# Kernel tuning notes

Measured on AMD Instinct MI355X. Metric: run time of the kernel, lower is better.

The kernel has to match this reference:

```python
import jax, jax.numpy as jnp
import numpy as np

B, S, H, E, K, D = 1, 4096, 1024, 8, 2, 2048

def setup_inputs() -> dict:
    key = jax.random.key(0)
    k1, k2, k3, k4, k5 = jax.random.split(key, 5)
    x = jax.random.normal(k1, (B, S, H), dtype=jnp.float32)
    attention_mask = jnp.ones((B, S), dtype=jnp.int32)
    expert_weights = jax.random.uniform(k2, (B, S, K), dtype=jnp.float32)
    # distinct top-K expert indices per token (torch code requires at most one match per token)
    r = jax.random.uniform(k3, (B, S, E))
    chosen_expert_indices = jnp.argsort(r, axis=-1)[..., :K].astype(jnp.int64)
    down_proj = jax.random.normal(k4, (E, H, D), dtype=jnp.float32)
    up_proj = jax.random.normal(k5, (E, D, H), dtype=jnp.float32)
    return {"x": x, "attention_mask": attention_mask, "expert_weights": expert_weights,
            "chosen_expert_indices": chosen_expert_indices, "down_proj": down_proj, "up_proj": up_proj}

def reference(x, attention_mask, expert_weights, chosen_expert_indices, down_proj, up_proj):
    b, s, h = x.shape
    e = down_proj.shape[0]
    xt = x.reshape(-1, h)                                   # [N,H]
    n = xt.shape[0]
    mask = attention_mask.reshape(n, 1).astype(x.dtype)     # [N,1]
    idx = chosen_expert_indices.reshape(n, -1)              # [N,K]
    w = expert_weights.reshape(n, -1)                       # [N,K]
    onehot = jax.nn.one_hot(idx, e, dtype=x.dtype)          # [N,K,E]
    # per-token routing weight for each expert (0 if not chosen), masked
    we = jnp.einsum('nk,nke->ne', w, onehot) * mask         # [N,E]
    hid = jax.nn.relu(jnp.einsum('nh,ehd->end', xt, down_proj))  # [E,N,D]
    y = jnp.einsum('end,edh->enh', hid, up_proj)            # [E,N,H]
    mlp = jnp.einsum('ne,enh->nh', we, y)                   # [N,H]
    out = xt + mlp                                          # residual (B==1 as in source)
    return out.reshape(b, s, h)
```

## Files before the change

### kernel.cpp

```cpp
#include <hip/hip_runtime.h>
#include <stdint.h>

#define NTOK 4096
#define HDIM 1024
#define DDIM 2048
#define NEXP 8
#define NASS 8192

typedef __attribute__((ext_vector_type(8))) short bf16x8;
typedef __attribute__((ext_vector_type(4))) float f32x4;

typedef __attribute__((address_space(1))) const unsigned int gu32;
typedef __attribute__((address_space(3))) unsigned int lu32;

#define BARRIER() asm volatile("s_barrier" ::: "memory")
#define WAIT_VM0() asm volatile("s_waitcnt vmcnt(0)" ::: "memory")

__device__ __forceinline__ void async16(void* lds, const void* g) {
  __builtin_amdgcn_global_load_lds((gu32*)(uintptr_t)g, (lu32*)(uintptr_t)lds, 16, 0, 0);
}

__device__ __forceinline__ unsigned short f2bf(float f) {
  unsigned int u = __float_as_uint(f);
  return (unsigned short)((u + 0x7fffu + ((u >> 16) & 1u)) >> 16);
}
__device__ __forceinline__ float bf2f(unsigned short u) {
  return __uint_as_float(((unsigned int)u) << 16);
}

__global__ __launch_bounds__(256) void k_cvt_x(const float* __restrict__ x,
                                               unsigned short* __restrict__ x16) {
  int i = blockIdx.x * 256 + threadIdx.x;
  float4 v = reinterpret_cast<const float4*>(x)[i];
  ushort4 o;
  o.x = f2bf(v.x); o.y = f2bf(v.y); o.z = f2bf(v.z); o.w = f2bf(v.w);
  reinterpret_cast<ushort4*>(x16)[i] = o;
}

__global__ __launch_bounds__(256) void k_transpose(const float* __restrict__ in,
                                                   unsigned short* __restrict__ out,
                                                   int R, int C) {
  __shared__ float t[32][33];
  const size_t mbase = (size_t)blockIdx.z * R * C;
  int tid = threadIdx.x;
  int r = tid >> 3, c4 = (tid & 7) * 4;
  int gr = blockIdx.y * 32 + r;
  int gc = blockIdx.x * 32 + c4;
  float4 v = *reinterpret_cast<const float4*>(in + mbase + (size_t)gr * C + gc);
  t[r][c4 + 0] = v.x; t[r][c4 + 1] = v.y; t[r][c4 + 2] = v.z; t[r][c4 + 3] = v.w;
  __syncthreads();
  int orow = blockIdx.x * 32 + r;
  int oc4  = blockIdx.y * 32 + c4;
  ushort4 o;
  o.x = f2bf(t[c4 + 0][r]); o.y = f2bf(t[c4 + 1][r]);
  o.z = f2bf(t[c4 + 2][r]); o.w = f2bf(t[c4 + 3][r]);
  *reinterpret_cast<ushort4*>(out + mbase + (size_t)orow * R + oc4) = o;
}

__global__ __launch_bounds__(1024) void k_route(
    const int* __restrict__ idx, const float* __restrict__ ew,
    const int* __restrict__ amask,
    int* __restrict__ counts_g, int* __restrict__ offs_g,
    int* __restrict__ toks, float* __restrict__ wl, int* __restrict__ slotmap) {
  __shared__ int cnt[NEXP], cur[NEXP], flag;
  const int t = threadIdx.x;
  if (t < NEXP) cnt[t] = 0;
  if (t == 0) flag = 0;
  __syncthreads();
  int lf = 0;
#pragma unroll
  for (int j = 0; j < 4; ++j) {
    int i = t + j * 1024;
    if (idx[2 * i + 1] != 0) lf = 1;
  }
  if (lf) atomicOr(&flag, 1);
  __syncthreads();
  const int is32 = flag;
  int e[8];
#pragma unroll
  for (int j = 0; j < 8; ++j) {
    int i = t + j * 1024;
    int ei = is32 ? idx[i] : idx[2 * i];
    e[j] = ei;
    atomicAdd(&cnt[ei], 1);
  }
  __syncthreads();
  if (t == 0) {
    int off = 0;
    for (int k = 0; k < NEXP; ++k) {
      cur[k] = off; offs_g[k] = off; counts_g[k] = cnt[k]; off += cnt[k];
    }
  }
  __syncthreads();
#pragma unroll
  for (int j = 0; j < 8; ++j) {
    int i = t + j * 1024;
    int n = i >> 1;
    int slot = atomicAdd(&cur[e[j]], 1);
    toks[slot] = n;
    wl[slot] = ew[i] * (amask[n] ? 1.0f : 0.0f);
    slotmap[i] = slot;
  }
}

__global__ __launch_bounds__(512, 4) void k_down_fused(
    const unsigned short* __restrict__ x16, const unsigned short* __restrict__ bT,
    const int* __restrict__ counts, const int* __restrict__ offs,
    const int* __restrict__ toks, unsigned short* __restrict__ hid,
    const float* __restrict__ up, unsigned short* __restrict__ upT) {
  const int e = blockIdx.x;
  const int q = blockIdx.y;
  const int tid = threadIdx.x;
  __shared__ alignas(16) char lds[65536];

  if (q >= 1024) {
    const int tt = (q - 1024) * 2 + (tid >> 8);
    const int bx = tt & 31;
    const int by = tt >> 5;
    float* tb = (float*)lds + (tid >> 8) * (32 * 33);
    const int t2 = tid & 255;
    const int r = t2 >> 3, c4 = (t2 & 7) * 4;
    const size_t mbase = (size_t)e * DDIM * HDIM;
    const int gr = by * 32 + r;
    const int gc = bx * 32 + c4;
    float4 v = *reinterpret_cast<const float4*>(up + mbase + (size_t)gr * HDIM + gc);
    tb[r * 33 + c4 + 0] = v.x; tb[r * 33 + c4 + 1] = v.y;
    tb[r * 33 + c4 + 2] = v.z; tb[r * 33 + c4 + 3] = v.w;
    __syncthreads();
    const int orow = bx * 32 + r;
    const int oc4  = by * 32 + c4;
    ushort4 o;
    o.x = f2bf(tb[(c4 + 0) * 33 + r]); o.y = f2bf(tb[(c4 + 1) * 33 + r]);
    o.z = f2bf(tb[(c4 + 2) * 33 + r]); o.w = f2bf(tb[(c4 + 3) * 33 + r]);
    *reinterpret_cast<ushort4*>(upT + mbase + (size_t)orow * DDIM + oc4) = o;
    return;
  }

  const int cnt = counts[e];
  const int mt = q >> 4;
  const int nt = q & 15;
  if (mt * 128 >= cnt) return;
  const int base = offs[e];
  const int lane = tid & 63;
  const int wr = ((tid >> 8) & 1) * 64;
  const int wc = ((tid >> 6) & 3) * 32;

  const char* gA[2]; const char* gB[2]; int sOff[2];
  {
    const int swcol = ((tid & 7) << 4) ^ (((tid >> 3) & 7) << 4);
#pragma unroll
    for (int it = 0; it < 2; ++it) {
      int row = it * 64 + (tid >> 3);
      int sl = mt * 128 + row; if (sl >= cnt) sl = cnt - 1;
      gA[it] = (const char*)(x16 + (size_t)toks[base + sl] * HDIM) + swcol;
      gB[it] = (const char*)(bT + (size_t)e * DDIM * HDIM + (size_t)(nt * 128 + row) * HDIM) + swcol;
      sOff[it] = it * 8192 + tid * 16;
    }
  }
  const int swz = (lane & 7) << 4;
  const int lo = (lane >> 4) << 4;
  int rowA[4], rowB[2];
#pragma unroll
  for (int m = 0; m < 4; ++m) rowA[m] = (wr + m * 16 + (lane & 15)) * 128;
#pragma unroll
  for (int n = 0; n < 2; ++n) rowB[n] = (wc + n * 16 + (lane & 15)) * 128;

#pragma unroll
  for (int it = 0; it < 2; ++it) {
    async16(lds + sOff[it], gA[it]);
    async16(lds + 32768 + sOff[it], gB[it]);
  }
  WAIT_VM0();
  BARRIER();

  f32x4 acc[4][2] = {};
  for (int j = 0; j < 16; ++j) {
    char* curA = lds + ((j & 1) << 14);
    char* curB = lds + 32768 + ((j & 1) << 14);
    char* nxtA = lds + ((~j & 1) << 14);
    char* nxtB = lds + 32768 + ((~j & 1) << 14);
    bf16x8 fa0[4], fb0[2], fa1[4], fb1[2];
    {
      const int cx = lo ^ swz;
#pragma unroll
      for (int m = 0; m < 4; ++m) fa0[m] = *reinterpret_cast<const bf16x8*>(curA + rowA[m] + cx);
#pragma unroll
      for (int n = 0; n < 2; ++n) fb0[n] = *reinterpret_cast<const bf16x8*>(curB + rowB[n] + cx);
    }
    if (j < 15) {
      const int ko = (j + 1) << 7;
#pragma unroll
      for (int it = 0; it < 2; ++it) {
        async16(nxtA + sOff[it], gA[it] + ko);
        async16(nxtB + sOff[it], gB[it] + ko);
      }
    }
    {
      const int cx = (64 | lo) ^ swz;
#pragma unroll
      for (int m = 0; m < 4; ++m) fa1[m] = *reinterpret_cast<const bf16x8*>(curA + rowA[m] + cx);
#pragma unroll
      for (int n = 0; n < 2; ++n) fb1[n] = *reinterpret_cast<const bf16x8*>(curB + rowB[n] + cx);
    }
#pragma unroll
    for (int m = 0; m < 4; ++m)
#pragma unroll
      for (int n = 0; n < 2; ++n)
        acc[m][n] = __builtin_amdgcn_mfma_f32_16x16x32_bf16(fa0[m], fb0[n], acc[m][n], 0, 0, 0);
#pragma unroll
    for (int m = 0; m < 4; ++m)
#pragma unroll
      for (int n = 0; n < 2; ++n)
        acc[m][n] = __builtin_amdgcn_mfma_f32_16x16x32_bf16(fa1[m], fb1[n], acc[m][n], 0, 0, 0);
    WAIT_VM0();
    BARRIER();
  }

#pragma unroll
  for (int m = 0; m < 4; ++m) {
    int r0 = mt * 128 + wr + m * 16 + ((lane >> 4) * 4);
#pragma unroll
    for (int j = 0; j < 4; ++j) {
      int r = r0 + j;
      if (r < cnt) {
        unsigned short* dst = hid + (size_t)(base + r) * DDIM + nt * 128 + wc + (lane & 15);
#pragma unroll
        for (int n = 0; n < 2; ++n) {
          float v = acc[m][n][j];
          dst[n * 16] = f2bf(v > 0.f ? v : 0.f);
        }
      }
    }
  }
}

__global__ __launch_bounds__(512, 4) void k_gemm_up(
    const unsigned short* __restrict__ hid, const unsigned short* __restrict__ bT,
    const int* __restrict__ counts, const int* __restrict__ offs,
    unsigned short* __restrict__ yw) {
  const int e = blockIdx.x;
  const int cnt = counts[e];
  const int q = blockIdx.y;
  const int mt = q >> 3;
  const int nt = q & 7;
  if (mt * 128 >= cnt) return;
  const int base = offs[e];
  __shared__ alignas(16) char lds[65536];
  const int tid = threadIdx.x;
  const int lane = tid & 63;
  const int wr = ((tid >> 8) & 1) * 64;
  const int wc = ((tid >> 6) & 3) * 32;

  const char* gA[2]; const char* gB[2]; int sOff[2];
  {
    const int swcol = ((tid & 7) << 4) ^ (((tid >> 3) & 7) << 4);
#pragma unroll
    for (int it = 0; it < 2; ++it) {
      int row = it * 64 + (tid >> 3);
      int sl = mt * 128 + row; if (sl >= cnt) sl = cnt - 1;
      gA[it] = (const char*)(hid + (size_t)(base + sl) * DDIM) + swcol;
      gB[it] = (const char*)(bT + (size_t)e * HDIM * DDIM + (size_t)(nt * 128 + row) * DDIM) + swcol;
      sOff[it] = it * 8192 + tid * 16;
    }
  }
  const int swz = (lane & 7) << 4;
  const int lo = (lane >> 4) << 4;
  int rowA[4], rowB[2];
#pragma unroll
  for (int m = 0; m < 4; ++m) rowA[m] = (wr + m * 16 + (lane & 15)) * 128;
#pragma unroll
  for (int n = 0; n < 2; ++n) rowB[n] = (wc + n * 16 + (lane & 15)) * 128;

#pragma unroll
  for (int it = 0; it < 2; ++it) {
    async16(lds + sOff[it], gA[it]);
    async16(lds + 32768 + sOff[it], gB[it]);
  }
  WAIT_VM0();
  BARRIER();

  f32x4 acc[4][2] = {};
  for (int j = 0; j < 32; ++j) {
    char* curA = lds + ((j & 1) << 14);
    char* curB = lds + 32768 + ((j & 1) << 14);
    char* nxtA = lds + ((~j & 1) << 14);
    char* nxtB = lds + 32768 + ((~j & 1) << 14);
    bf16x8 fa0[4], fb0[2], fa1[4], fb1[2];
    {
      const int cx = lo ^ swz;
#pragma unroll
      for (int m = 0; m < 4; ++m) fa0[m] = *reinterpret_cast<const bf16x8*>(curA + rowA[m] + cx);
#pragma unroll
      for (int n = 0; n < 2; ++n) fb0[n] = *reinterpret_cast<const bf16x8*>(curB + rowB[n] + cx);
    }
    if (j < 31) {
      const int ko = (j + 1) << 7;
#pragma unroll
      for (int it = 0; it < 2; ++it) {
        async16(nxtA + sOff[it], gA[it] + ko);
        async16(nxtB + sOff[it], gB[it] + ko);
      }
    }
    {
      const int cx = (64 | lo) ^ swz;
#pragma unroll
      for (int m = 0; m < 4; ++m) fa1[m] = *reinterpret_cast<const bf16x8*>(curA + rowA[m] + cx);
#pragma unroll
      for (int n = 0; n < 2; ++n) fb1[n] = *reinterpret_cast<const bf16x8*>(curB + rowB[n] + cx);
    }
#pragma unroll
    for (int m = 0; m < 4; ++m)
#pragma unroll
      for (int n = 0; n < 2; ++n)
        acc[m][n] = __builtin_amdgcn_mfma_f32_16x16x32_bf16(fa0[m], fb0[n], acc[m][n], 0, 0, 0);
#pragma unroll
    for (int m = 0; m < 4; ++m)
#pragma unroll
      for (int n = 0; n < 2; ++n)
        acc[m][n] = __builtin_amdgcn_mfma_f32_16x16x32_bf16(fa1[m], fb1[n], acc[m][n], 0, 0, 0);
    WAIT_VM0();
    BARRIER();
  }

#pragma unroll
  for (int m = 0; m < 4; ++m) {
    int r0 = mt * 128 + wr + m * 16 + ((lane >> 4) * 4);
#pragma unroll
    for (int j = 0; j < 4; ++j) {
      int r = r0 + j;
      if (r < cnt) {
        unsigned short* dst = yw + (size_t)(base + r) * HDIM + nt * 128 + wc + (lane & 15);
#pragma unroll
        for (int n = 0; n < 2; ++n) dst[n * 16] = f2bf(acc[m][n][j]);
      }
    }
  }
}

__global__ __launch_bounds__(256) void k_combine(
    const float* __restrict__ x, const unsigned short* __restrict__ yw,
    const int* __restrict__ slotmap, const float* __restrict__ wl,
    float* __restrict__ out) {
  const int n = blockIdx.x;
  const int t = threadIdx.x;
  const int s0 = slotmap[2 * n], s1 = slotmap[2 * n + 1];
  const float w0 = wl[s0], w1 = wl[s1];
  float4 xv = reinterpret_cast<const float4*>(x + (size_t)n * HDIM)[t];
  ushort4 a0 = reinterpret_cast<const ushort4*>(yw + (size_t)s0 * HDIM)[t];
  ushort4 b0 = reinterpret_cast<const ushort4*>(yw + (size_t)s1 * HDIM)[t];
  float4 r;
  r.x = xv.x + w0 * bf2f(a0.x) + w1 * bf2f(b0.x);
  r.y = xv.y + w0 * bf2f(a0.y) + w1 * bf2f(b0.y);
  r.z = xv.z + w0 * bf2f(a0.z) + w1 * bf2f(b0.z);
  r.w = xv.w + w0 * bf2f(a0.w) + w1 * bf2f(b0.w);
  reinterpret_cast<float4*>(out + (size_t)n * HDIM)[t] = r;
}

extern "C" void kernel_launch(void* const* d_in, const int* in_sizes, int n_in,
                              void* d_out, int out_size, void* d_ws, size_t ws_size,
                              hipStream_t stream) {
  const float* x    = (const float*)d_in[0];
  const int* amask  = (const int*)d_in[1];
  const float* ew   = (const float*)d_in[2];
  const int* cidx   = (const int*)d_in[3];
  const float* dn   = (const float*)d_in[4];
  const float* up   = (const float*)d_in[5];
  float* out        = (float*)d_out;
  char* ws          = (char*)d_ws;

  const size_t X16_OFF = 0;
  const size_t DNT_OFF = X16_OFF + (size_t)NTOK * HDIM * 2;
  const size_t UPT_OFF = DNT_OFF + (size_t)NEXP * HDIM * DDIM * 2;
  const size_t HID_OFF = UPT_OFF + (size_t)NEXP * HDIM * DDIM * 2;
  const size_t MET_OFF = HID_OFF + (size_t)NASS * DDIM * 2;

  unsigned short* x16 = (unsigned short*)(ws + X16_OFF);
  unsigned short* dnT = (unsigned short*)(ws + DNT_OFF);
  unsigned short* upT = (unsigned short*)(ws + UPT_OFF);
  unsigned short* hid = (unsigned short*)(ws + HID_OFF);
  unsigned short* yw  = (unsigned short*)(ws + DNT_OFF);
  int* counts  = (int*)(ws + MET_OFF);
  int* offs    = counts + 8;
  int* toks    = counts + 32;
  float* wl    = (float*)(toks + NASS);
  int* slotmap = (int*)(wl + NASS);

  k_cvt_x<<<NTOK * HDIM / 1024, 256, 0, stream>>>(x, x16);
  k_transpose<<<dim3(DDIM / 32, HDIM / 32, NEXP), 256, 0, stream>>>(dn, dnT, HDIM, DDIM);
  k_route<<<1, 1024, 0, stream>>>(cidx, ew, amask, counts, offs, toks, wl, slotmap);
  k_down_fused<<<dim3(8, 2048), 512, 0, stream>>>(x16, dnT, counts, offs, toks, hid,
                                                  up, upT);
  k_gemm_up<<<dim3(8, 512), 512, 0, stream>>>(hid, upT, counts, offs, yw);
  k_combine<<<NTOK, 256, 0, stream>>>(x, yw, slotmap, wl, out);
}
```

Before: 159.8 us.

## Triple-buffer GEMM K-loop with prefetch depth two and unfuse up-proj transpose

Both expert GEMM kernels move from a double-buffered LDS pipeline that waited for all loads at the end of each iteration to a three-stage ring. Loads are issued two k-steps ahead and the wait uses vmcnt(4), so memory latency can overlap more of the MFMA work. LDS per block grows to 96KB and launch bounds drop to two blocks per CU, which lowers occupancy. The up_proj transpose that had been fused into the down GEMM launch now runs as its own transpose kernel, so it no longer overlaps with the GEMM.

```diff
diff --git a/kernel.cpp b/kernel.cpp
--- a/kernel.cpp
+++ b/kernel.cpp
@@ -14,7 +14,6 @@
 typedef __attribute__((address_space(3))) unsigned int lu32;
 
 #define BARRIER() asm volatile("s_barrier" ::: "memory")
-#define WAIT_VM0() asm volatile("s_waitcnt vmcnt(0)" ::: "memory")
 
 __device__ __forceinline__ void async16(void* lds, const void* g) {
   __builtin_amdgcn_global_load_lds((gu32*)(uintptr_t)g, (lu32*)(uintptr_t)lds, 16, 0, 0);
@@ -103,44 +102,19 @@
   }
 }
 
-__global__ __launch_bounds__(512, 4) void k_down_fused(
+__global__ __launch_bounds__(512, 2) void k_gemm_down(
     const unsigned short* __restrict__ x16, const unsigned short* __restrict__ bT,
     const int* __restrict__ counts, const int* __restrict__ offs,
-    const int* __restrict__ toks, unsigned short* __restrict__ hid,
-    const float* __restrict__ up, unsigned short* __restrict__ upT) {
+    const int* __restrict__ toks, unsigned short* __restrict__ hid) {
   const int e = blockIdx.x;
+  const int cnt = counts[e];
   const int q = blockIdx.y;
-  const int tid = threadIdx.x;
-  __shared__ alignas(16) char lds[65536];
-
-  if (q >= 1024) {
-    const int tt = (q - 1024) * 2 + (tid >> 8);
-    const int bx = tt & 31;
-    const int by = tt >> 5;
-    float* tb = (float*)lds + (tid >> 8) * (32 * 33);
-    const int t2 = tid & 255;
-    const int r = t2 >> 3, c4 = (t2 & 7) * 4;
-    const size_t mbase = (size_t)e * DDIM * HDIM;
-    const int gr = by * 32 + r;
-    const int gc = bx * 32 + c4;
-    float4 v = *reinterpret_cast<const float4*>(up + mbase + (size_t)gr * HDIM + gc);
-    tb[r * 33 + c4 + 0] = v.x; tb[r * 33 + c4 + 1] = v.y;
-    tb[r * 33 + c4 + 2] = v.z; tb[r * 33 + c4 + 3] = v.w;
-    __syncthreads();
-    const int orow = bx * 32 + r;
-    const int oc4  = by * 32 + c4;
-    ushort4 o;
-    o.x = f2bf(tb[(c4 + 0) * 33 + r]); o.y = f2bf(tb[(c4 + 1) * 33 + r]);
-    o.z = f2bf(tb[(c4 + 2) * 33 + r]); o.w = f2bf(tb[(c4 + 3) * 33 + r]);
-    *reinterpret_cast<ushort4*>(upT + mbase + (size_t)orow * DDIM + oc4) = o;
-    return;
-  }
-
-  const int cnt = counts[e];
   const int mt = q >> 4;
   const int nt = q & 15;
   if (mt * 128 >= cnt) return;
   const int base = offs[e];
+  __shared__ alignas(16) char lds[98304];
+  const int tid = threadIdx.x;
   const int lane = tid & 63;
   const int wr = ((tid >> 8) & 1) * 64;
   const int wc = ((tid >> 6) & 3) * 32;
@@ -168,17 +142,32 @@
 #pragma unroll
   for (int it = 0; it < 2; ++it) {
     async16(lds + sOff[it], gA[it]);
-    async16(lds + 32768 + sOff[it], gB[it]);
-  }
-  WAIT_VM0();
-  BARRIER();
+    async16(lds + 49152 + sOff[it], gB[it]);
+  }
+#pragma unroll
+  for (int it = 0; it < 2; ++it) {
+    async16(lds + 16384 + sOff[it], gA[it] + 128);
+    async16(lds + 49152 + 16384 + sOff[it], gB[it] + 128);
+  }
 
   f32x4 acc[4][2] = {};
+  int cj = 0, sj = 2;
   for (int j = 0; j < 16; ++j) {
-    char* curA = lds + ((j & 1) << 14);
-    char* curB = lds + 32768 + ((j & 1) << 14);
-    char* nxtA = lds + ((~j & 1) << 14);
-    char* nxtB = lds + 32768 + ((~j & 1) << 14);
+    if (j < 15) { asm volatile("s_waitcnt vmcnt(4)" ::: "memory"); }
+    else        { asm volatile("s_waitcnt vmcnt(0)" ::: "memory"); }
+    BARRIER();
+    if (j + 2 < 16) {
+      const int ko = (j + 2) << 7;
+      char* sA = lds + sj * 16384;
+      char* sB = lds + 49152 + sj * 16384;
+#pragma unroll
+      for (int it = 0; it < 2; ++it) {
+        async16(sA + sOff[it], gA[it] + ko);
+        async16(sB + sOff[it], gB[it] + ko);
+      }
+    }
+    char* curA = lds + cj * 16384;
+    char* curB = lds + 49152 + cj * 16384;
     bf16x8 fa0[4], fb0[2], fa1[4], fb1[2];
     {
       const int cx = lo ^ swz;
@@ -187,14 +176,6 @@
 #pragma unroll
       for (int n = 0; n < 2; ++n) fb0[n] = *reinterpret_cast<const bf16x8*>(curB + rowB[n] + cx);
     }
-    if (j < 15) {
-      const int ko = (j + 1) << 7;
-#pragma unroll
-      for (int it = 0; it < 2; ++it) {
-        async16(nxtA + sOff[it], gA[it] + ko);
-        async16(nxtB + sOff[it], gB[it] + ko);
-      }
-    }
     {
       const int cx = (64 | lo) ^ swz;
 #pragma unroll
@@ -212,8 +193,8 @@
 #pragma unroll
       for (int n = 0; n < 2; ++n)
         acc[m][n] = __builtin_amdgcn_mfma_f32_16x16x32_bf16(fa1[m], fb1[n], acc[m][n], 0, 0, 0);
-    WAIT_VM0();
-    BARRIER();
+    cj = (cj == 2) ? 0 : cj + 1;
+    sj = (sj == 2) ? 0 : sj + 1;
   }
 
 #pragma unroll
@@ -234,7 +215,7 @@
   }
 }
 
-__global__ __launch_bounds__(512, 4) void k_gemm_up(
+__global__ __launch_bounds__(512, 2) void k_gemm_up(
     const unsigned short* __restrict__ hid, const unsigned short* __restrict__ bT,
     const int* __restrict__ counts, const int* __restrict__ offs,
     unsigned short* __restrict__ yw) {
@@ -245,7 +226,7 @@
   const int nt = q & 7;
   if (mt * 128 >= cnt) return;
   const int base = offs[e];
-  __shared__ alignas(16) char lds[65536];
+  __shared__ alignas(16) char lds[98304];
   const int tid = threadIdx.x;
   const int lane = tid & 63;
   const int wr = ((tid >> 8) & 1) * 64;
@@ -274,17 +255,32 @@
 #pragma unroll
   for (int it = 0; it < 2; ++it) {
     async16(lds + sOff[it], gA[it]);
-    async16(lds + 32768 + sOff[it], gB[it]);
-  }
-  WAIT_VM0();
-  BARRIER();
+    async16(lds + 49152 + sOff[it], gB[it]);
+  }
+#pragma unroll
+  for (int it = 0; it < 2; ++it) {
+    async16(lds + 16384 + sOff[it], gA[it] + 128);
+    async16(lds + 49152 + 16384 + sOff[it], gB[it] + 128);
+  }
 
   f32x4 acc[4][2] = {};
+  int cj = 0, sj = 2;
   for (int j = 0; j < 32; ++j) {
-    char* curA = lds + ((j & 1) << 14);
-    char* curB = lds + 32768 + ((j & 1) << 14);
-    char* nxtA = lds + ((~j & 1) << 14);
-    char* nxtB = lds + 32768 + ((~j & 1) << 14);
+    if (j < 31) { asm volatile("s_waitcnt vmcnt(4)" ::: "memory"); }
+    else        { asm volatile("s_waitcnt vmcnt(0)" ::: "memory"); }
+    BARRIER();
+    if (j + 2 < 32) {
+      const int ko = (j + 2) << 7;
+      char* sA = lds + sj * 16384;
+      char* sB = lds + 49152 + sj * 16384;
+#pragma unroll
+      for (int it = 0; it < 2; ++it) {
+        async16(sA + sOff[it], gA[it] + ko);
+        async16(sB + sOff[it], gB[it] + ko);
+      }
+    }
+    char* curA = lds + cj * 16384;
+    char* curB = lds + 49152 + cj * 16384;
     bf16x8 fa0[4], fb0[2], fa1[4], fb1[2];
     {
       const int cx = lo ^ swz;
@@ -293,14 +289,6 @@
 #pragma unroll
       for (int n = 0; n < 2; ++n) fb0[n] = *reinterpret_cast<const bf16x8*>(curB + rowB[n] + cx);
     }
-    if (j < 31) {
-      const int ko = (j + 1) << 7;
-#pragma unroll
-      for (int it = 0; it < 2; ++it) {
-        async16(nxtA + sOff[it], gA[it] + ko);
-        async16(nxtB + sOff[it], gB[it] + ko);
-      }
-    }
     {
       const int cx = (64 | lo) ^ swz;
 #pragma unroll
@@ -318,8 +306,8 @@
 #pragma unroll
       for (int n = 0; n < 2; ++n)
         acc[m][n] = __builtin_amdgcn_mfma_f32_16x16x32_bf16(fa1[m], fb1[n], acc[m][n], 0, 0, 0);
-    WAIT_VM0();
-    BARRIER();
+    cj = (cj == 2) ? 0 : cj + 1;
+    sj = (sj == 2) ? 0 : sj + 1;
   }
 
 #pragma unroll
@@ -387,9 +375,9 @@
 
   k_cvt_x<<<NTOK * HDIM / 1024, 256, 0, stream>>>(x, x16);
   k_transpose<<<dim3(DDIM / 32, HDIM / 32, NEXP), 256, 0, stream>>>(dn, dnT, HDIM, DDIM);
+  k_transpose<<<dim3(HDIM / 32, DDIM / 32, NEXP), 256, 0, stream>>>(up, upT, DDIM, HDIM);
   k_route<<<1, 1024, 0, stream>>>(cidx, ew, amask, counts, offs, toks, wl, slotmap);
-  k_down_fused<<<dim3(8, 2048), 512, 0, stream>>>(x16, dnT, counts, offs, toks, hid,
-                                                  up, upT);
+  k_gemm_down<<<dim3(8, 1024), 512, 0, stream>>>(x16, dnT, counts, offs, toks, hid);
   k_gemm_up<<<dim3(8, 512), 512, 0, stream>>>(hid, upT, counts, offs, yw);
   k_combine<<<NTOK, 256, 0, stream>>>(x, yw, slotmap, wl, out);
 }
```

New measurement: 165.7 us. 1.04x slower.
